# Optimization experiments

Measured on AMD Instinct MI355X. Metric: run time of the kernel, lower is better.

## Reference

```python
import jax, jax.numpy as jnp
import numpy as np

N = 50000        # nodes
E = 800000       # edges (avg degree 16)
F = 64           # num_features
G = 128          # number of graphs in the batch
NOUT = 1         # n_output


def setup_inputs() -> dict:
    key = jax.random.key(0)
    ks = jax.random.split(key, 9)
    x = jax.random.normal(ks[0], (N, F), dtype=jnp.float32)
    edge_index = jax.random.randint(ks[1], (2, E), 0, N, dtype=jnp.int64)
    batch = jnp.sort(jax.random.randint(ks[2], (N,), 0, G, dtype=jnp.int64))
    W1 = jax.random.normal(ks[3], (F, F), dtype=jnp.float32) * 0.1
    b1 = jnp.zeros((F,), dtype=jnp.float32)
    W2 = jax.random.normal(ks[4], (F, 2 * F), dtype=jnp.float32) * 0.1
    b2 = jnp.zeros((2 * F,), dtype=jnp.float32)
    fcW = jax.random.normal(ks[5], (2 * F, NOUT), dtype=jnp.float32) * 0.1
    fcb = jnp.zeros((NOUT,), dtype=jnp.float32)
    return {"x": x, "edge_index": edge_index, "batch": batch,
            "W1": W1, "b1": b1, "W2": W2, "b2": b2, "fcW": fcW, "fcb": fcb}


def reference(x, edge_index, batch, W1, b1, W2, b2, fcW, fcb):
    n = x.shape[0]
    # PyG GCNConv: add self-loops, symmetric normalization D^-1/2 (A+I) D^-1/2
    loop = jnp.arange(n, dtype=edge_index.dtype)
    src = jnp.concatenate([edge_index[0], loop])  # [E+N]
    dst = jnp.concatenate([edge_index[1], loop])  # [E+N]
    deg = jax.ops.segment_sum(jnp.ones_like(dst, dtype=x.dtype), dst, num_segments=n)
    dinv = jnp.where(deg > 0, jax.lax.rsqrt(jnp.maximum(deg, 1.0)), 0.0)
    norm = dinv[src] * dinv[dst]                  # [E+N]

    def gcn_conv(h, W, b):
        h = h @ W                                 # [N, Fout]
        msg = h[src] * norm[:, None]              # gather + scale, [E+N, Fout]
        return jax.ops.segment_sum(msg, dst, num_segments=n) + b

    h1 = jax.nn.relu(gcn_conv(x, W1, b1))         # [N, F]
    h2 = jax.nn.relu(gcn_conv(h1, W2, b2))        # [N, 2F]

    # global mean pool per graph (dropout is identity in eval)
    counts = jax.ops.segment_sum(jnp.ones((n,), x.dtype), batch, num_segments=G)
    pooled = jax.ops.segment_sum(h2, batch, num_segments=G)
    pooled = pooled / jnp.maximum(counts, 1.0)[:, None]  # [G, 2F]

    out = pooled @ fcW + fcb                      # [G, NOUT]
    return out.reshape(1, -1)                     # [1, G*NOUT]
```

## Files before the change

kernel.cpp:

```cpp
#include <hip/hip_runtime.h>
#include <hip/hip_bf16.h>

typedef __hip_bfloat16 bf16;

static __device__ __forceinline__ float loadF(const void* p, long long i, int f32){
  return f32 ? ((const float*)p)[i] : __bfloat162float(((const bf16*)p)[i]);
}
static __device__ __forceinline__ int loadI(const void* p, long long i, int i64){
  return i64 ? (int)((const long long*)p)[i] : ((const int*)p)[i];
}
static __device__ __forceinline__ unsigned short f2bf(float f){
  unsigned u = __float_as_uint(f);
  return (unsigned short)((u + 0x7FFFu + ((u>>16)&1u)) >> 16);
}
static __device__ __forceinline__ float bf2f(unsigned v){
  return __uint_as_float(v<<16);
}

#define CAP 4096
#define LB_EDGES 8192

__global__ void k_init(const unsigned int* __restrict__ xw, const unsigned int* __restrict__ eiw,
                       int* __restrict__ flags, int* __restrict__ gcursor, int nbuckets,
                       float* __restrict__ S, int gn){
  int i = blockIdx.x*256 + threadIdx.x;
  if(i < nbuckets) gcursor[i] = 0;
  if(i < gn) S[i] = 0.f;
  if(blockIdx.x == 0){
    __shared__ int s1, s2;
    if(threadIdx.x==0){ s1=0; s2=0; }
    __syncthreads();
    unsigned w = xw[threadIdx.x];
    int e = (int)((w>>7)&0xFFu);
    if(e>=110 && e<=135) atomicAdd(&s1, 1);
    if(eiw[2*threadIdx.x+1] != 0u) atomicAdd(&s2, 1);
    __syncthreads();
    if(threadIdx.x==0){
      flags[0] = (s1 < 128) ? 1 : 0;
      flags[1] = (s2 < 128) ? 1 : 0;
    }
  }
}

__global__ __launch_bounds__(256) void k_pre(const void* __restrict__ ei, int E, int N,
                                             const int* __restrict__ flags,
                                             int* __restrict__ gcursor,
                                             unsigned int* __restrict__ log, int nbuckets,
                                             const void* __restrict__ x, const void* __restrict__ W,
                                             unsigned short* __restrict__ y, int nLog){
  __shared__ unsigned int smem[12416];
  int t = threadIdx.x;
  if((int)blockIdx.x < nLog){
    unsigned int* stash = smem;
    int* hcnt  = (int*)(smem + LB_EDGES);
    int* hbase = (int*)(smem + LB_EDGES + 1024);
    for(int b=t; b<nbuckets; b+=256) hcnt[b] = 0;
    __syncthreads();
    int i64 = flags[1];
    long long e0 = (long long)blockIdx.x*LB_EDGES;
    int cnt = (int)(((long long)E - e0) < LB_EDGES ? ((long long)E - e0) : LB_EDGES);
    for(int k=t; k<cnt; k+=256){
      long long e = e0 + k;
      int s = loadI(ei, e, i64);                 s = min(max(s,0), N-1);
      int d = loadI(ei, (long long)E + e, i64);  d = min(max(d,0), N-1);
      unsigned p = (((unsigned)d)<<16) | (unsigned)s;
      stash[k] = p;
      atomicAdd(&hcnt[d>>6], 1);
    }
    __syncthreads();
    for(int b=t; b<nbuckets; b+=256){
      int c = hcnt[b];
      hbase[b] = (c>0) ? atomicAdd(&gcursor[b], c) : 0;
      hcnt[b] = 0;
    }
    __syncthreads();
    for(int k=t; k<cnt; k+=256){
      unsigned p = stash[k];
      int b = (int)(p>>22);
      int pos = hbase[b] + atomicAdd(&hcnt[b], 1);
      if(pos < CAP) log[(long long)b*CAP + pos] = p;
    }
  } else {
    float* Ws = (float*)smem;
    float* xs = (float*)(smem + 4096);
    int f32 = flags[0];
    for(int i=t;i<4096;i+=256) Ws[i] = loadF(W, i, f32);
    int row0 = ((int)blockIdx.x - nLog)*128;
    for(int i=t;i<8192;i+=256){
      int r = i>>6, c = i&63;
      int gr = row0 + r;
      xs[r*65 + c] = (gr<N) ? loadF(x, (long long)gr*64 + c, f32) : 0.f;
    }
    __syncthreads();
    int cg = t&15, rg = t>>4;
    int col_g = cg*4, row_g = rg*8;
    float acc[8][4];
    #pragma unroll
    for(int r=0;r<8;r++){ acc[r][0]=0.f; acc[r][1]=0.f; acc[r][2]=0.f; acc[r][3]=0.f; }
    for(int k=0;k<64;k++){
      float4 w = *(const float4*)&Ws[k*64 + col_g];
      float xr[8];
      #pragma unroll
      for(int r=0;r<8;r++) xr[r] = xs[(row_g+r)*65 + k];
      #pragma unroll
      for(int r=0;r<8;r++){
        acc[r][0] += xr[r]*w.x; acc[r][1] += xr[r]*w.y;
        acc[r][2] += xr[r]*w.z; acc[r][3] += xr[r]*w.w;
      }
    }
    #pragma unroll
    for(int r=0;r<8;r++){
      int gr = row0 + row_g + r;
      if(gr<N){
        ushort4 st;
        st.x = f2bf(acc[r][0]); st.y = f2bf(acc[r][1]);
        st.z = f2bf(acc[r][2]); st.w = f2bf(acc[r][3]);
        *(ushort4*)&y[(long long)gr*64 + col_g] = st;
      }
    }
  }
}

__global__ __launch_bounds__(256) void k_bsortg0(const unsigned int* __restrict__ log,
                                                 const int* __restrict__ gcursor,
                                                 unsigned short* __restrict__ csr,
                                                 int* __restrict__ beg, int* __restrict__ endv,
                                                 float* __restrict__ dinv,
                                                 const unsigned int* __restrict__ Y32,
                                                 unsigned int* __restrict__ G032, int N){
  __shared__ int hist[64];
  __shared__ int cur[64];
  __shared__ float dloc[64];
  int b = blockIdx.x, t = threadIdx.x;
  if(t < 64) hist[t] = 0;
  __syncthreads();
  int n = min(gcursor[b], CAP);
  const unsigned int* L = log + (long long)b*CAP;
  for(int j=t; j<n; j+=256) atomicAdd(&hist[(L[j]>>16)&63], 1);
  __syncthreads();
  if(t < 64){
    int v = hist[t];
    int inc = v;
    #pragma unroll
    for(int o=1; o<64; o<<=1){
      int u = __shfl_up(inc, o);
      if(t >= o) inc += u;
    }
    int excl = inc - v;
    cur[t] = excl;
    float dv = rsqrtf((float)(v + 1));
    dloc[t] = dv;
    int node = b*64 + t;
    if(node < N){
      int base = b*CAP + excl;
      beg[node]  = base;
      endv[node] = base + v;
      dinv[node] = dv;
    }
  }
  __syncthreads();
  unsigned short* C = csr + (long long)b*CAP;
  for(int j=t; j<n; j+=256){
    unsigned p = L[j];
    int l = (int)((p>>16)&63u);
    int pos = atomicAdd(&cur[l], 1);
    C[pos] = (unsigned short)(p & 0xFFFFu);
  }
  long long base32 = (long long)b*2048;
  for(int i=t; i<2048; i+=256){
    int nl = i>>5;
    int node = b*64 + nl;
    if(node < N){
      unsigned v = Y32[base32 + i];
      float dv = dloc[nl];
      G032[base32 + i] = (unsigned)f2bf(bf2f(v & 0xFFFFu)*dv)
                       | ((unsigned)f2bf(bf2f(v >> 16)*dv) << 16);
    }
  }
}

__global__ __launch_bounds__(256) void k_agg(const unsigned short* __restrict__ g,
                                             const unsigned short* __restrict__ csr,
                                             const int* __restrict__ beg, const int* __restrict__ endv,
                                             const float* __restrict__ dinv,
                                             const void* __restrict__ bias, const int* __restrict__ flags,
                                             int mode,
                                             unsigned int* __restrict__ out32, int N){
  int node = blockIdx.x*4 + (threadIdx.x>>6);
  int lane = threadIdx.x&63;
  if(node >= N) return;
  int half = lane>>5, fl = lane&31;
  const unsigned int* G32 = (const unsigned int*)g;
  int j = beg[node], e = endv[node];
  float2 a0={0.f,0.f}, a1={0.f,0.f}, a2={0.f,0.f}, a3={0.f,0.f};
  float2 a4={0.f,0.f}, a5={0.f,0.f}, a6={0.f,0.f}, a7={0.f,0.f};
  for(; j+16<=e; j+=16){
    int s0 = csr[j +  0 + half];
    int s1 = csr[j +  2 + half];
    int s2 = csr[j +  4 + half];
    int s3 = csr[j +  6 + half];
    int s4 = csr[j +  8 + half];
    int s5 = csr[j + 10 + half];
    int s6 = csr[j + 12 + half];
    int s7 = csr[j + 14 + half];
    unsigned v0 = G32[(long long)s0*32 + fl];
    unsigned v1 = G32[(long long)s1*32 + fl];
    unsigned v2 = G32[(long long)s2*32 + fl];
    unsigned v3 = G32[(long long)s3*32 + fl];
    unsigned v4 = G32[(long long)s4*32 + fl];
    unsigned v5 = G32[(long long)s5*32 + fl];
    unsigned v6 = G32[(long long)s6*32 + fl];
    unsigned v7 = G32[(long long)s7*32 + fl];
    a0.x += bf2f(v0 & 0xFFFFu); a0.y += bf2f(v0 >> 16);
    a1.x += bf2f(v1 & 0xFFFFu); a1.y += bf2f(v1 >> 16);
    a2.x += bf2f(v2 & 0xFFFFu); a2.y += bf2f(v2 >> 16);
    a3.x += bf2f(v3 & 0xFFFFu); a3.y += bf2f(v3 >> 16);
    a4.x += bf2f(v4 & 0xFFFFu); a4.y += bf2f(v4 >> 16);
    a5.x += bf2f(v5 & 0xFFFFu); a5.y += bf2f(v5 >> 16);
    a6.x += bf2f(v6 & 0xFFFFu); a6.y += bf2f(v6 >> 16);
    a7.x += bf2f(v7 & 0xFFFFu); a7.y += bf2f(v7 >> 16);
  }
  for(; j+8<=e; j+=8){
    int s0 = csr[j + 0 + half];
    int s1 = csr[j + 2 + half];
    int s2 = csr[j + 4 + half];
    int s3 = csr[j + 6 + half];
    unsigned v0 = G32[(long long)s0*32 + fl];
    unsigned v1 = G32[(long long)s1*32 + fl];
    unsigned v2 = G32[(long long)s2*32 + fl];
    unsigned v3 = G32[(long long)s3*32 + fl];
    a0.x += bf2f(v0 & 0xFFFFu); a0.y += bf2f(v0 >> 16);
    a1.x += bf2f(v1 & 0xFFFFu); a1.y += bf2f(v1 >> 16);
    a2.x += bf2f(v2 & 0xFFFFu); a2.y += bf2f(v2 >> 16);
    a3.x += bf2f(v3 & 0xFFFFu); a3.y += bf2f(v3 >> 16);
  }
  for(; j+2<=e; j+=2){
    int s = csr[j + half];
    unsigned v = G32[(long long)s*32 + fl];
    a0.x += bf2f(v & 0xFFFFu); a0.y += bf2f(v >> 16);
  }
  if(j < e && half == 0){
    int s = csr[j];
    unsigned v = G32[(long long)s*32 + fl];
    a0.x += bf2f(v & 0xFFFFu); a0.y += bf2f(v >> 16);
  }
  float sx = ((a0.x+a1.x)+(a2.x+a3.x)) + ((a4.x+a5.x)+(a6.x+a7.x));
  float sy = ((a0.y+a1.y)+(a2.y+a3.y)) + ((a4.y+a5.y)+(a6.y+a7.y));
  sx += __shfl_xor(sx, 32, 64);
  sy += __shfl_xor(sy, 32, 64);
  unsigned sv = G32[(long long)node*32 + fl];
  float dv = dinv[node];
  sx = (sx + bf2f(sv & 0xFFFFu)) * dv;
  sy = (sy + bf2f(sv >> 16)) * dv;
  if(mode){
    int f32 = flags[0];
    float bx = loadF(bias, 2*fl,   f32);
    float by = loadF(bias, 2*fl+1, f32);
    sx = fmaxf(sx + bx, 0.f) * dv;
    sy = fmaxf(sy + by, 0.f) * dv;
  }
  if(half == 0)
    out32[(long long)node*32 + fl] = (unsigned)f2bf(sx) | ((unsigned)f2bf(sy) << 16);
}

__global__ __launch_bounds__(256) void k_gemm2pool(const unsigned int* __restrict__ A32, const void* __restrict__ W,
                                                   const void* __restrict__ b, const void* __restrict__ fcW,
                                                   const void* __restrict__ batch, const int* __restrict__ flags,
                                                   float* __restrict__ S, int N, int NOUT){
  __shared__ float Ws[64*128];
  __shared__ float xs[128*65];
  __shared__ float Sloc[128*4];
  __shared__ int gid[128];
  int f32 = flags[0], i64 = flags[1];
  int tid = threadIdx.x;
  int row0 = blockIdx.x*128;
  for(int i=tid;i<8192;i+=256) Ws[i] = loadF(W, i, f32);
  for(int i=tid;i<4096;i+=256){
    int r = i>>5, kd = i&31;
    int gr = row0 + r;
    unsigned v = (gr<N) ? A32[(long long)gr*32 + kd] : 0u;
    xs[r*65 + 2*kd    ] = bf2f(v & 0xFFFFu);
    xs[r*65 + 2*kd + 1] = bf2f(v >> 16);
  }
  if(tid < 128){
    int node = row0 + tid;
    gid[tid] = (node < N) ? loadI(batch, node, i64) : 0;
  }
  for(int i=tid;i<512;i+=256) Sloc[i] = 0.f;
  __syncthreads();
  int cg = tid&15, rg = tid>>4;
  int c0 = cg*4, c1 = 64 + cg*4, row_g = rg*8;
  float acc[8][8];
  #pragma unroll
  for(int r=0;r<8;r++)
    #pragma unroll
    for(int c=0;c<8;c++) acc[r][c]=0.f;
  for(int k=0;k<64;k++){
    float4 w0 = *(const float4*)&Ws[k*128 + c0];
    float4 w1 = *(const float4*)&Ws[k*128 + c1];
    float xr[8];
    #pragma unroll
    for(int r=0;r<8;r++) xr[r] = xs[(row_g+r)*65 + k];
    #pragma unroll
    for(int r=0;r<8;r++){
      acc[r][0] += xr[r]*w0.x; acc[r][1] += xr[r]*w0.y;
      acc[r][2] += xr[r]*w0.z; acc[r][3] += xr[r]*w0.w;
      acc[r][4] += xr[r]*w1.x; acc[r][5] += xr[r]*w1.y;
      acc[r][6] += xr[r]*w1.z; acc[r][7] += xr[r]*w1.w;
    }
  }
  #pragma unroll
  for(int c=0;c<8;c++){
    int col = (c<4) ? (c0+c) : (c1+c-4);
    float bb = loadF(b, col, f32);
    #pragma unroll
    for(int r=0;r<8;r++){ float z = acc[r][c]+bb; acc[r][c] = z>0.f?z:0.f; }
  }
  int nv = N - row0; nv = nv < 128 ? nv : 128;
  if(nv <= 0) return;
  int gmin = gid[0], gmax = gid[nv-1];
  bool ldsOK = (NOUT <= 4) && (gmax - gmin < 128);
  for(int o=0;o<NOUT;o++){
    float fw[8];
    #pragma unroll
    for(int c=0;c<8;c++){
      int col = (c<4) ? (c0+c) : (c1+c-4);
      fw[c] = loadF(fcW, (long long)col*NOUT + o, f32);
    }
    #pragma unroll
    for(int r=0;r<8;r++){
      float z = acc[r][0]*fw[0] + acc[r][1]*fw[1] + acc[r][2]*fw[2] + acc[r][3]*fw[3]
              + acc[r][4]*fw[4] + acc[r][5]*fw[5] + acc[r][6]*fw[6] + acc[r][7]*fw[7];
      #pragma unroll
      for(int m=1;m<16;m<<=1) z += __shfl_xor(z, m, 64);
      int nl = row_g + r;
      if(cg==0 && nl < nv){
        int gg = gid[nl];
        if(ldsOK) atomicAdd(&Sloc[(gg-gmin)*NOUT + o], z);
        else      atomicAdd(&S[(long long)gg*NOUT + o], z);
      }
    }
  }
  if(ldsOK){
    __syncthreads();
    int nbin = (gmax - gmin + 1)*NOUT;
    for(int i=tid; i<nbin; i+=256){
      float v = Sloc[i];
      if(v != 0.f){
        int bin = i / NOUT, o = i - bin*NOUT;
        atomicAdd(&S[(long long)(gmin+bin)*NOUT + o], v);
      }
    }
  }
}

static __device__ __forceinline__ int lower_bound_batch(const void* batch, int N, int key, int i64){
  int lo = 0, hi = N;
  while(lo < hi){ int mid = (lo+hi)>>1; if(loadI(batch, mid, i64) < key) lo = mid+1; else hi = mid; }
  return lo;
}

__global__ void k_final2(const float* __restrict__ S, const void* __restrict__ batch, int N,
                         const int* __restrict__ flags, const void* __restrict__ fcb,
                         void* __restrict__ out, int G, int NOUT){
  int f32 = flags[0], i64 = flags[1];
  int g = blockIdx.x*256 + threadIdx.x;
  if(g >= G) return;
  int c = lower_bound_batch(batch, N, g+1, i64) - lower_bound_batch(batch, N, g, i64);
  float inv = 1.f / (float)(c > 0 ? c : 1);
  for(int o=0;o<NOUT;o++){
    float r = S[(long long)g*NOUT+o]*inv + loadF(fcb, o, f32);
    if(f32) ((float*)out)[g*NOUT+o] = r;
    else    ((unsigned short*)out)[g*NOUT+o] = f2bf(r);
  }
}

extern "C" void kernel_launch(void* const* d_in, const int* in_sizes, int n_in,
                              void* d_out, int out_size, void* d_ws, size_t ws_size,
                              hipStream_t stream) {
  const void* x    = d_in[0];
  const void* ei   = d_in[1];
  const void* batch= d_in[2];
  const void* W1   = d_in[3];
  const void* b1   = d_in[4];
  const void* W2   = d_in[5];
  const void* b2   = d_in[6];
  const void* fcW  = d_in[7];
  const void* fcb  = d_in[8];

  const int N = in_sizes[0] / 64;
  const int E = in_sizes[1] / 2;
  const int NOUT = in_sizes[8];
  const int G = out_size / NOUT;
  const int nbuckets = (N + 63) >> 6;

  size_t off = 0;
  auto alloc = [&](size_t bytes) -> char* {
    char* p = (char*)d_ws + off;
    off += (bytes + 511) & ~(size_t)511;
    return p;
  };
  int*   flags   = (int*)  alloc(512);
  int*   gcursor = (int*)  alloc((size_t)nbuckets*4);
  float* dinv    = (float*)alloc((size_t)N*4);
  int*   beg     = (int*)  alloc((size_t)N*4);
  int*   endv    = (int*)  alloc((size_t)N*4);
  float* S       = (float*)alloc((size_t)G*NOUT*4);
  unsigned int*   log  = (unsigned int*)  alloc((size_t)nbuckets*CAP*4);
  unsigned short* csr  = (unsigned short*)alloc((size_t)nbuckets*CAP*2);
  unsigned short* yB   = (unsigned short*)alloc((size_t)N*64*2);
  unsigned short* g0   = (unsigned short*)alloc((size_t)N*64*2);
  unsigned short* g1   = (unsigned short*)alloc((size_t)N*64*2);
  unsigned int*   aBuf = (unsigned int*)  alloc((size_t)N*32*4);
  (void)ws_size; (void)n_in;

  int initgrid = (nbuckets > G*NOUT ? nbuckets : G*NOUT);
  int nLog = (E + LB_EDGES - 1) / LB_EDGES;
  int nGem = (N + 127) / 128;

  k_init    <<<(initgrid+255)/256, 256, 0, stream>>>((const unsigned int*)x, (const unsigned int*)ei,
                                                     flags, gcursor, nbuckets, S, G*NOUT);
  k_pre     <<<nLog + nGem,   256, 0, stream>>>(ei, E, N, flags, gcursor, log, nbuckets,
                                                x, W1, yB, nLog);
  k_bsortg0 <<<nbuckets,      256, 0, stream>>>(log, gcursor, csr, beg, endv, dinv,
                                                (const unsigned int*)yB, (unsigned int*)g0, N);

  k_agg     <<<(N+3)/4,       256, 0, stream>>>(g0, csr, beg, endv, dinv, b1, flags, 1,
                                                (unsigned int*)g1, N);
  k_agg     <<<(N+3)/4,       256, 0, stream>>>(g1, csr, beg, endv, dinv, b1, flags, 0,
                                                aBuf, N);
  k_gemm2pool<<<(N+127)/128,  256, 0, stream>>>(aBuf, W2, b2, fcW, batch, flags, S, N, NOUT);

  k_final2  <<<(G+255)/256,   256, 0, stream>>>(S, batch, N, flags, fcb, d_out, G, NOUT);
}
```

Measured before the change: 203.7 us.

## Fuse second aggregation into GEMM2/pool kernel and fold final reduction via last-block

Measured after the change: 250.0 us. +22.7%, slower.

```diff
diff --git a/kernel.cpp b/kernel.cpp
--- a/kernel.cpp
+++ b/kernel.cpp
@@ -22,10 +22,11 @@
 
 __global__ void k_init(const unsigned int* __restrict__ xw, const unsigned int* __restrict__ eiw,
                        int* __restrict__ flags, int* __restrict__ gcursor, int nbuckets,
-                       float* __restrict__ S, int gn){
+                       float* __restrict__ S, int gn, int* __restrict__ done){
   int i = blockIdx.x*256 + threadIdx.x;
   if(i < nbuckets) gcursor[i] = 0;
   if(i < gn) S[i] = 0.f;
+  if(i == 0) done[0] = 0;
   if(blockIdx.x == 0){
     __shared__ int s1, s2;
     if(threadIdx.x==0){ s1=0; s2=0; }
@@ -84,12 +85,32 @@
     float* Ws = (float*)smem;
     float* xs = (float*)(smem + 4096);
     int f32 = flags[0];
-    for(int i=t;i<4096;i+=256) Ws[i] = loadF(W, i, f32);
     int row0 = ((int)blockIdx.x - nLog)*128;
-    for(int i=t;i<8192;i+=256){
-      int r = i>>6, c = i&63;
-      int gr = row0 + r;
-      xs[r*65 + c] = (gr<N) ? loadF(x, (long long)gr*64 + c, f32) : 0.f;
+    if(f32){
+      const float4* W4 = (const float4*)W;
+      for(int i=t;i<1024;i+=256){
+        float4 v = W4[i];
+        Ws[i*4]=v.x; Ws[i*4+1]=v.y; Ws[i*4+2]=v.z; Ws[i*4+3]=v.w;
+      }
+      const float4* X4 = (const float4*)x;
+      for(int i=t;i<2048;i+=256){
+        int r = i>>4, c4 = i&15;
+        int gr = row0 + r;
+        float4 v = {0.f,0.f,0.f,0.f};
+        if(gr<N) v = X4[(long long)gr*16 + c4];
+        float* xd = &xs[r*65 + c4*4];
+        xd[0]=v.x; xd[1]=v.y; xd[2]=v.z; xd[3]=v.w;
+      }
+    } else {
+      for(int i=t;i<4096;i+=256) Ws[i] = loadF(W, i, 0);
+      const unsigned int* X32 = (const unsigned int*)x;
+      for(int i=t;i<4096;i+=256){
+        int r = i>>5, kd = i&31;
+        int gr = row0 + r;
+        unsigned v = (gr<N) ? X32[(long long)gr*32 + kd] : 0u;
+        xs[r*65 + 2*kd    ] = bf2f(v & 0xFFFFu);
+        xs[r*65 + 2*kd + 1] = bf2f(v >> 16);
+      }
     }
     __syncthreads();
     int cg = t&15, rg = t>>4;
@@ -121,16 +142,13 @@
   }
 }
 
-__global__ __launch_bounds__(256) void k_bsortg0(const unsigned int* __restrict__ log,
-                                                 const int* __restrict__ gcursor,
-                                                 unsigned short* __restrict__ csr,
-                                                 int* __restrict__ beg, int* __restrict__ endv,
-                                                 float* __restrict__ dinv,
-                                                 const unsigned int* __restrict__ Y32,
-                                                 unsigned int* __restrict__ G032, int N){
+__global__ __launch_bounds__(256) void k_bsort(const unsigned int* __restrict__ log,
+                                               const int* __restrict__ gcursor,
+                                               unsigned short* __restrict__ csr,
+                                               int* __restrict__ beg, int* __restrict__ endv,
+                                               float* __restrict__ dinv, int N){
   __shared__ int hist[64];
   __shared__ int cur[64];
-  __shared__ float dloc[64];
   int b = blockIdx.x, t = threadIdx.x;
   if(t < 64) hist[t] = 0;
   __syncthreads();
@@ -148,14 +166,12 @@
     }
     int excl = inc - v;
     cur[t] = excl;
-    float dv = rsqrtf((float)(v + 1));
-    dloc[t] = dv;
     int node = b*64 + t;
     if(node < N){
       int base = b*CAP + excl;
       beg[node]  = base;
       endv[node] = base + v;
-      dinv[node] = dv;
+      dinv[node] = rsqrtf((float)(v + 1));
     }
   }
   __syncthreads();
@@ -166,31 +182,19 @@
     int pos = atomicAdd(&cur[l], 1);
     C[pos] = (unsigned short)(p & 0xFFFFu);
   }
-  long long base32 = (long long)b*2048;
-  for(int i=t; i<2048; i+=256){
-    int nl = i>>5;
-    int node = b*64 + nl;
-    if(node < N){
-      unsigned v = Y32[base32 + i];
-      float dv = dloc[nl];
-      G032[base32 + i] = (unsigned)f2bf(bf2f(v & 0xFFFFu)*dv)
-                       | ((unsigned)f2bf(bf2f(v >> 16)*dv) << 16);
-    }
-  }
-}
-
-__global__ __launch_bounds__(256) void k_agg(const unsigned short* __restrict__ g,
-                                             const unsigned short* __restrict__ csr,
-                                             const int* __restrict__ beg, const int* __restrict__ endv,
-                                             const float* __restrict__ dinv,
-                                             const void* __restrict__ bias, const int* __restrict__ flags,
-                                             int mode,
-                                             unsigned int* __restrict__ out32, int N){
+}
+
+__global__ __launch_bounds__(256) void k_agg1(const unsigned short* __restrict__ yB,
+                                              const unsigned short* __restrict__ csr,
+                                              const int* __restrict__ beg, const int* __restrict__ endv,
+                                              const float* __restrict__ dinv,
+                                              const void* __restrict__ bias, const int* __restrict__ flags,
+                                              unsigned int* __restrict__ out32, int N){
   int node = blockIdx.x*4 + (threadIdx.x>>6);
   int lane = threadIdx.x&63;
   if(node >= N) return;
   int half = lane>>5, fl = lane&31;
-  const unsigned int* G32 = (const unsigned int*)g;
+  const unsigned int* G32 = (const unsigned int*)yB;
   int j = beg[node], e = endv[node];
   float2 a0={0.f,0.f}, a1={0.f,0.f}, a2={0.f,0.f}, a3={0.f,0.f};
   float2 a4={0.f,0.f}, a5={0.f,0.f}, a6={0.f,0.f}, a7={0.f,0.f};
@@ -203,6 +207,8 @@
     int s5 = csr[j + 10 + half];
     int s6 = csr[j + 12 + half];
     int s7 = csr[j + 14 + half];
+    float d0 = dinv[s0], d1 = dinv[s1], d2 = dinv[s2], d3 = dinv[s3];
+    float d4 = dinv[s4], d5 = dinv[s5], d6 = dinv[s6], d7 = dinv[s7];
     unsigned v0 = G32[(long long)s0*32 + fl];
     unsigned v1 = G32[(long long)s1*32 + fl];
     unsigned v2 = G32[(long long)s2*32 + fl];
@@ -211,38 +217,41 @@
     unsigned v5 = G32[(long long)s5*32 + fl];
     unsigned v6 = G32[(long long)s6*32 + fl];
     unsigned v7 = G32[(long long)s7*32 + fl];
-    a0.x += bf2f(v0 & 0xFFFFu); a0.y += bf2f(v0 >> 16);
-    a1.x += bf2f(v1 & 0xFFFFu); a1.y += bf2f(v1 >> 16);
-    a2.x += bf2f(v2 & 0xFFFFu); a2.y += bf2f(v2 >> 16);
-    a3.x += bf2f(v3 & 0xFFFFu); a3.y += bf2f(v3 >> 16);
-    a4.x += bf2f(v4 & 0xFFFFu); a4.y += bf2f(v4 >> 16);
-    a5.x += bf2f(v5 & 0xFFFFu); a5.y += bf2f(v5 >> 16);
-    a6.x += bf2f(v6 & 0xFFFFu); a6.y += bf2f(v6 >> 16);
-    a7.x += bf2f(v7 & 0xFFFFu); a7.y += bf2f(v7 >> 16);
+    a0.x += d0*bf2f(v0 & 0xFFFFu); a0.y += d0*bf2f(v0 >> 16);
+    a1.x += d1*bf2f(v1 & 0xFFFFu); a1.y += d1*bf2f(v1 >> 16);
+    a2.x += d2*bf2f(v2 & 0xFFFFu); a2.y += d2*bf2f(v2 >> 16);
+    a3.x += d3*bf2f(v3 & 0xFFFFu); a3.y += d3*bf2f(v3 >> 16);
+    a4.x += d4*bf2f(v4 & 0xFFFFu); a4.y += d4*bf2f(v4 >> 16);
+    a5.x += d5*bf2f(v5 & 0xFFFFu); a5.y += d5*bf2f(v5 >> 16);
+    a6.x += d6*bf2f(v6 & 0xFFFFu); a6.y += d6*bf2f(v6 >> 16);
+    a7.x += d7*bf2f(v7 & 0xFFFFu); a7.y += d7*bf2f(v7 >> 16);
   }
   for(; j+8<=e; j+=8){
     int s0 = csr[j + 0 + half];
     int s1 = csr[j + 2 + half];
     int s2 = csr[j + 4 + half];
     int s3 = csr[j + 6 + half];
+    float d0 = dinv[s0], d1 = dinv[s1], d2 = dinv[s2], d3 = dinv[s3];
     unsigned v0 = G32[(long long)s0*32 + fl];
     unsigned v1 = G32[(long long)s1*32 + fl];
     unsigned v2 = G32[(long long)s2*32 + fl];
     unsigned v3 = G32[(long long)s3*32 + fl];
-    a0.x += bf2f(v0 & 0xFFFFu); a0.y += bf2f(v0 >> 16);
-    a1.x += bf2f(v1 & 0xFFFFu); a1.y += bf2f(v1 >> 16);
-    a2.x += bf2f(v2 & 0xFFFFu); a2.y += bf2f(v2 >> 16);
-    a3.x += bf2f(v3 & 0xFFFFu); a3.y += bf2f(v3 >> 16);
+    a0.x += d0*bf2f(v0 & 0xFFFFu); a0.y += d0*bf2f(v0 >> 16);
+    a1.x += d1*bf2f(v1 & 0xFFFFu); a1.y += d1*bf2f(v1 >> 16);
+    a2.x += d2*bf2f(v2 & 0xFFFFu); a2.y += d2*bf2f(v2 >> 16);
+    a3.x += d3*bf2f(v3 & 0xFFFFu); a3.y += d3*bf2f(v3 >> 16);
   }
   for(; j+2<=e; j+=2){
     int s = csr[j + half];
+    float d = dinv[s];
     unsigned v = G32[(long long)s*32 + fl];
-    a0.x += bf2f(v & 0xFFFFu); a0.y += bf2f(v >> 16);
+    a0.x += d*bf2f(v & 0xFFFFu); a0.y += d*bf2f(v >> 16);
   }
   if(j < e && half == 0){
     int s = csr[j];
+    float d = dinv[s];
     unsigned v = G32[(long long)s*32 + fl];
-    a0.x += bf2f(v & 0xFFFFu); a0.y += bf2f(v >> 16);
+    a0.x += d*bf2f(v & 0xFFFFu); a0.y += d*bf2f(v >> 16);
   }
   float sx = ((a0.x+a1.x)+(a2.x+a3.x)) + ((a4.x+a5.x)+(a6.x+a7.x));
   float sy = ((a0.y+a1.y)+(a2.y+a3.y)) + ((a4.y+a5.y)+(a6.y+a7.y));
@@ -250,43 +259,122 @@
   sy += __shfl_xor(sy, 32, 64);
   unsigned sv = G32[(long long)node*32 + fl];
   float dv = dinv[node];
-  sx = (sx + bf2f(sv & 0xFFFFu)) * dv;
-  sy = (sy + bf2f(sv >> 16)) * dv;
-  if(mode){
-    int f32 = flags[0];
-    float bx = loadF(bias, 2*fl,   f32);
-    float by = loadF(bias, 2*fl+1, f32);
-    sx = fmaxf(sx + bx, 0.f) * dv;
-    sy = fmaxf(sy + by, 0.f) * dv;
-  }
+  sx = (sx + dv*bf2f(sv & 0xFFFFu)) * dv;
+  sy = (sy + dv*bf2f(sv >> 16)) * dv;
+  int f32 = flags[0];
+  float bx = loadF(bias, 2*fl,   f32);
+  float by = loadF(bias, 2*fl+1, f32);
+  sx = fmaxf(sx + bx, 0.f) * dv;
+  sy = fmaxf(sy + by, 0.f) * dv;
   if(half == 0)
     out32[(long long)node*32 + fl] = (unsigned)f2bf(sx) | ((unsigned)f2bf(sy) << 16);
 }
 
-__global__ __launch_bounds__(256) void k_gemm2pool(const unsigned int* __restrict__ A32, const void* __restrict__ W,
-                                                   const void* __restrict__ b, const void* __restrict__ fcW,
-                                                   const void* __restrict__ batch, const int* __restrict__ flags,
-                                                   float* __restrict__ S, int N, int NOUT){
+static __device__ __forceinline__ int lower_bound_batch(const void* batch, int N, int key, int i64){
+  int lo = 0, hi = N;
+  while(lo < hi){ int mid = (lo+hi)>>1; if(loadI(batch, mid, i64) < key) lo = mid+1; else hi = mid; }
+  return lo;
+}
+
+__global__ __launch_bounds__(256) void k_gemm2agg(const unsigned short* __restrict__ g1,
+                                                  const unsigned short* __restrict__ csr,
+                                                  const int* __restrict__ beg, const int* __restrict__ endv,
+                                                  const float* __restrict__ dinv,
+                                                  const void* __restrict__ W, const void* __restrict__ b,
+                                                  const void* __restrict__ fcW, const void* __restrict__ batch,
+                                                  const int* __restrict__ flags,
+                                                  float* __restrict__ S, int* __restrict__ done,
+                                                  const void* __restrict__ fcb, void* __restrict__ out,
+                                                  int N, int G, int NOUT){
   __shared__ float Ws[64*128];
   __shared__ float xs[128*65];
   __shared__ float Sloc[128*4];
   __shared__ int gid[128];
+  __shared__ int lastBlk;
   int f32 = flags[0], i64 = flags[1];
   int tid = threadIdx.x;
   int row0 = blockIdx.x*128;
   for(int i=tid;i<8192;i+=256) Ws[i] = loadF(W, i, f32);
-  for(int i=tid;i<4096;i+=256){
-    int r = i>>5, kd = i&31;
-    int gr = row0 + r;
-    unsigned v = (gr<N) ? A32[(long long)gr*32 + kd] : 0u;
-    xs[r*65 + 2*kd    ] = bf2f(v & 0xFFFFu);
-    xs[r*65 + 2*kd + 1] = bf2f(v >> 16);
-  }
   if(tid < 128){
     int node = row0 + tid;
     gid[tid] = (node < N) ? loadI(batch, node, i64) : 0;
   }
   for(int i=tid;i<512;i+=256) Sloc[i] = 0.f;
+  {
+    const unsigned int* G32 = (const unsigned int*)g1;
+    int w = tid>>6, lane = tid&63, half = lane>>5, fl = lane&31;
+    for(int r = w*32; r < w*32 + 32; ++r){
+      int node = row0 + r;
+      float sx = 0.f, sy = 0.f;
+      if(node < N){
+        int j = beg[node], e = endv[node];
+        float2 a0={0.f,0.f}, a1={0.f,0.f}, a2={0.f,0.f}, a3={0.f,0.f};
+        float2 a4={0.f,0.f}, a5={0.f,0.f}, a6={0.f,0.f}, a7={0.f,0.f};
+        for(; j+16<=e; j+=16){
+          int s0 = csr[j +  0 + half];
+          int s1 = csr[j +  2 + half];
+          int s2 = csr[j +  4 + half];
+          int s3 = csr[j +  6 + half];
+          int s4 = csr[j +  8 + half];
+          int s5 = csr[j + 10 + half];
+          int s6 = csr[j + 12 + half];
+          int s7 = csr[j + 14 + half];
+          unsigned v0 = G32[(long long)s0*32 + fl];
+          unsigned v1 = G32[(long long)s1*32 + fl];
+          unsigned v2 = G32[(long long)s2*32 + fl];
+          unsigned v3 = G32[(long long)s3*32 + fl];
+          unsigned v4 = G32[(long long)s4*32 + fl];
+          unsigned v5 = G32[(long long)s5*32 + fl];
+          unsigned v6 = G32[(long long)s6*32 + fl];
+          unsigned v7 = G32[(long long)s7*32 + fl];
+          a0.x += bf2f(v0 & 0xFFFFu); a0.y += bf2f(v0 >> 16);
+          a1.x += bf2f(v1 & 0xFFFFu); a1.y += bf2f(v1 >> 16);
+          a2.x += bf2f(v2 & 0xFFFFu); a2.y += bf2f(v2 >> 16);
+          a3.x += bf2f(v3 & 0xFFFFu); a3.y += bf2f(v3 >> 16);
+          a4.x += bf2f(v4 & 0xFFFFu); a4.y += bf2f(v4 >> 16);
+          a5.x += bf2f(v5 & 0xFFFFu); a5.y += bf2f(v5 >> 16);
+          a6.x += bf2f(v6 & 0xFFFFu); a6.y += bf2f(v6 >> 16);
+          a7.x += bf2f(v7 & 0xFFFFu); a7.y += bf2f(v7 >> 16);
+        }
+        for(; j+8<=e; j+=8){
+          int s0 = csr[j + 0 + half];
+          int s1 = csr[j + 2 + half];
+          int s2 = csr[j + 4 + half];
+          int s3 = csr[j + 6 + half];
+          unsigned v0 = G32[(long long)s0*32 + fl];
+          unsigned v1 = G32[(long long)s1*32 + fl];
+          unsigned v2 = G32[(long long)s2*32 + fl];
+          unsigned v3 = G32[(long long)s3*32 + fl];
+          a0.x += bf2f(v0 & 0xFFFFu); a0.y += bf2f(v0 >> 16);
+          a1.x += bf2f(v1 & 0xFFFFu); a1.y += bf2f(v1 >> 16);
+          a2.x += bf2f(v2 & 0xFFFFu); a2.y += bf2f(v2 >> 16);
+          a3.x += bf2f(v3 & 0xFFFFu); a3.y += bf2f(v3 >> 16);
+        }
+        for(; j+2<=e; j+=2){
+          int s = csr[j + half];
+          unsigned v = G32[(long long)s*32 + fl];
+          a0.x += bf2f(v & 0xFFFFu); a0.y += bf2f(v >> 16);
+        }
+        if(j < e && half == 0){
+          int s = csr[j];
+          unsigned v = G32[(long long)s*32 + fl];
+          a0.x += bf2f(v & 0xFFFFu); a0.y += bf2f(v >> 16);
+        }
+        sx = ((a0.x+a1.x)+(a2.x+a3.x)) + ((a4.x+a5.x)+(a6.x+a7.x));
+        sy = ((a0.y+a1.y)+(a2.y+a3.y)) + ((a4.y+a5.y)+(a6.y+a7.y));
+        sx += __shfl_xor(sx, 32, 64);
+        sy += __shfl_xor(sy, 32, 64);
+        unsigned sv = G32[(long long)node*32 + fl];
+        float dv = dinv[node];
+        sx = (sx + bf2f(sv & 0xFFFFu)) * dv;
+        sy = (sy + bf2f(sv >> 16)) * dv;
+      }
+      if(half == 0){
+        xs[r*65 + 2*fl    ] = sx;
+        xs[r*65 + 2*fl + 1] = sy;
+      }
+    }
+  }
   __syncthreads();
   int cg = tid&15, rg = tid>>4;
   int c0 = cg*4, c1 = 64 + cg*4, row_g = rg*8;
@@ -317,61 +405,57 @@
     for(int r=0;r<8;r++){ float z = acc[r][c]+bb; acc[r][c] = z>0.f?z:0.f; }
   }
   int nv = N - row0; nv = nv < 128 ? nv : 128;
-  if(nv <= 0) return;
-  int gmin = gid[0], gmax = gid[nv-1];
-  bool ldsOK = (NOUT <= 4) && (gmax - gmin < 128);
-  for(int o=0;o<NOUT;o++){
-    float fw[8];
-    #pragma unroll
-    for(int c=0;c<8;c++){
-      int col = (c<4) ? (c0+c) : (c1+c-4);
-      fw[c] = loadF(fcW, (long long)col*NOUT + o, f32);
-    }
-    #pragma unroll
-    for(int r=0;r<8;r++){
-      float z = acc[r][0]*fw[0] + acc[r][1]*fw[1] + acc[r][2]*fw[2] + acc[r][3]*fw[3]
-              + acc[r][4]*fw[4] + acc[r][5]*fw[5] + acc[r][6]*fw[6] + acc[r][7]*fw[7];
+  if(nv > 0){
+    int gmin = gid[0], gmax = gid[nv-1];
+    bool ldsOK = (NOUT <= 4) && (gmax - gmin < 128);
+    for(int o=0;o<NOUT;o++){
+      float fw[8];
       #pragma unroll
-      for(int m=1;m<16;m<<=1) z += __shfl_xor(z, m, 64);
-      int nl = row_g + r;
-      if(cg==0 && nl < nv){
-        int gg = gid[nl];
-        if(ldsOK) atomicAdd(&Sloc[(gg-gmin)*NOUT + o], z);
-        else      atomicAdd(&S[(long long)gg*NOUT + o], z);
-      }
-    }
-  }
-  if(ldsOK){
-    __syncthreads();
-    int nbin = (gmax - gmin + 1)*NOUT;
-    for(int i=tid; i<nbin; i+=256){
-      float v = Sloc[i];
-      if(v != 0.f){
-        int bin = i / NOUT, o = i - bin*NOUT;
-        atomicAdd(&S[(long long)(gmin+bin)*NOUT + o], v);
-      }
-    }
-  }
-}
-
-static __device__ __forceinline__ int lower_bound_batch(const void* batch, int N, int key, int i64){
-  int lo = 0, hi = N;
-  while(lo < hi){ int mid = (lo+hi)>>1; if(loadI(batch, mid, i64) < key) lo = mid+1; else hi = mid; }
-  return lo;
-}
-
-__global__ void k_final2(const float* __restrict__ S, const void* __restrict__ batch, int N,
-                         const int* __restrict__ flags, const void* __restrict__ fcb,
-                         void* __restrict__ out, int G, int NOUT){
-  int f32 = flags[0], i64 = flags[1];
-  int g = blockIdx.x*256 + threadIdx.x;
-  if(g >= G) return;
-  int c = lower_bound_batch(batch, N, g+1, i64) - lower_bound_batch(batch, N, g, i64);
-  float inv = 1.f / (float)(c > 0 ? c : 1);
-  for(int o=0;o<NOUT;o++){
-    float r = S[(long long)g*NOUT+o]*inv + loadF(fcb, o, f32);
-    if(f32) ((float*)out)[g*NOUT+o] = r;
-    else    ((unsigned short*)out)[g*NOUT+o] = f2bf(r);
+      for(int c=0;c<8;c++){
+        int col = (c<4) ? (c0+c) : (c1+c-4);
+        fw[c] = loadF(fcW, (long long)col*NOUT + o, f32);
+      }
+      #pragma unroll
+      for(int r=0;r<8;r++){
+        float z = acc[r][0]*fw[0] + acc[r][1]*fw[1] + acc[r][2]*fw[2] + acc[r][3]*fw[3]
+                + acc[r][4]*fw[4] + acc[r][5]*fw[5] + acc[r][6]*fw[6] + acc[r][7]*fw[7];
+        #pragma unroll
+        for(int m=1;m<16;m<<=1) z += __shfl_xor(z, m, 64);
+        int nl = row_g + r;
+        if(cg==0 && nl < nv){
+          int gg = gid[nl];
+          if(ldsOK) atomicAdd(&Sloc[(gg-gmin)*NOUT + o], z);
+          else      atomicAdd(&S[(long long)gg*NOUT + o], z);
+        }
+      }
+    }
+    if(ldsOK){
+      __syncthreads();
+      int nbin = (gmax - gmin + 1)*NOUT;
+      for(int i=tid; i<nbin; i+=256){
+        float v = Sloc[i];
+        if(v != 0.f){
+          int bin = i / NOUT, o = i - bin*NOUT;
+          atomicAdd(&S[(long long)(gmin+bin)*NOUT + o], v);
+        }
+      }
+    }
+  }
+  __threadfence();
+  if(tid==0) lastBlk = (atomicAdd(done, 1) == (int)gridDim.x - 1) ? 1 : 0;
+  __syncthreads();
+  if(lastBlk){
+    __threadfence();
+    for(int g2=tid; g2<G; g2+=256){
+      int c = lower_bound_batch(batch, N, g2+1, i64) - lower_bound_batch(batch, N, g2, i64);
+      float inv = 1.f / (float)(c > 0 ? c : 1);
+      for(int o=0;o<NOUT;o++){
+        float sv = atomicAdd(&S[(long long)g2*NOUT + o], 0.f);
+        float r = sv*inv + loadF(fcb, o, f32);
+        if(f32) ((float*)out)[g2*NOUT+o] = r;
+        else    ((unsigned short*)out)[g2*NOUT+o] = f2bf(r);
+      }
+    }
   }
 }
 
@@ -401,6 +485,7 @@
     return p;
   };
   int*   flags   = (int*)  alloc(512);
+  int*   done    = (int*)  alloc(512);
   int*   gcursor = (int*)  alloc((size_t)nbuckets*4);
   float* dinv    = (float*)alloc((size_t)N*4);
   int*   beg     = (int*)  alloc((size_t)N*4);
@@ -409,9 +494,7 @@
   unsigned int*   log  = (unsigned int*)  alloc((size_t)nbuckets*CAP*4);
   unsigned short* csr  = (unsigned short*)alloc((size_t)nbuckets*CAP*2);
   unsigned short* yB   = (unsigned short*)alloc((size_t)N*64*2);
-  unsigned short* g0   = (unsigned short*)alloc((size_t)N*64*2);
   unsigned short* g1   = (unsigned short*)alloc((size_t)N*64*2);
-  unsigned int*   aBuf = (unsigned int*)  alloc((size_t)N*32*4);
   (void)ws_size; (void)n_in;
 
   int initgrid = (nbuckets > G*NOUT ? nbuckets : G*NOUT);
@@ -419,17 +502,12 @@
   int nGem = (N + 127) / 128;
 
   k_init    <<<(initgrid+255)/256, 256, 0, stream>>>((const unsigned int*)x, (const unsigned int*)ei,
-                                                     flags, gcursor, nbuckets, S, G*NOUT);
+                                                     flags, gcursor, nbuckets, S, G*NOUT, done);
   k_pre     <<<nLog + nGem,   256, 0, stream>>>(ei, E, N, flags, gcursor, log, nbuckets,
                                                 x, W1, yB, nLog);
-  k_bsortg0 <<<nbuckets,      256, 0, stream>>>(log, gcursor, csr, beg, endv, dinv,
-                                                (const unsigned int*)yB, (unsigned int*)g0, N);
-
-  k_agg     <<<(N+3)/4,       256, 0, stream>>>(g0, csr, beg, endv, dinv, b1, flags, 1,
+  k_bsort   <<<nbuckets,      256, 0, stream>>>(log, gcursor, csr, beg, endv, dinv, N);
+  k_agg1    <<<(N+3)/4,       256, 0, stream>>>(yB, csr, beg, endv, dinv, b1, flags,
                                                 (unsigned int*)g1, N);
-  k_agg     <<<(N+3)/4,       256, 0, stream>>>(g1, csr, beg, endv, dinv, b1, flags, 0,
-                                                aBuf, N);
-  k_gemm2pool<<<(N+127)/128,  256, 0, stream>>>(aBuf, W2, b2, fcW, batch, flags, S, N, NOUT);
-
-  k_final2  <<<(G+255)/256,   256, 0, stream>>>(S, batch, N, flags, fcb, d_out, G, NOUT);
-}
+  k_gemm2agg<<<(N+127)/128,   256, 0, stream>>>(g1, csr, beg, endv, dinv, W2, b2, fcW, batch, flags,
+                                                S, done, fcb, d_out, N, G, NOUT);
+}
```
